# Performance work log

Hardware: AMD Instinct MI355X
Metric: run time of the kernel (lower is better)

## Reference

```python
import jax, jax.numpy as jnp
import numpy as np

B, S, F, H = 256, 1024, 64, 64

def setup_inputs() -> dict:
    key = jax.random.key(0)
    ks = jax.random.split(key, 6)
    x = jax.random.normal(ks[0], (B, S, F), dtype=jnp.float32)
    # Keras LSTM params: kernel [F,4H], recurrent_kernel [H,4H], bias [4H] (gate order i,f,c,o)
    kernel = jax.random.normal(ks[1], (F, 4 * H), dtype=jnp.float32) * (1.0 / np.sqrt(F))
    rec_kernel = jax.random.normal(ks[2], (H, 4 * H), dtype=jnp.float32) * (1.0 / np.sqrt(H))
    bias = jnp.zeros((4 * H,), dtype=jnp.float32)
    dense_w = jax.random.normal(ks[3], (H, 1), dtype=jnp.float32) * (1.0 / np.sqrt(H))
    dense_b = jnp.zeros((1,), dtype=jnp.float32)
    return {"x": x, "kernel": kernel, "rec_kernel": rec_kernel, "bias": bias,
            "dense_w": dense_w, "dense_b": dense_b}

def reference(x, kernel, rec_kernel, bias, dense_w, dense_b):
    # Precompute input contribution for all timesteps: [B,S,4H]
    xz = jnp.einsum('bsf,fg->bsg', x, kernel) + bias
    xz_t = jnp.transpose(xz, (1, 0, 2))  # [S,B,4H]

    def step(carry, xz_step):
        h, c = carry
        z = xz_step + h @ rec_kernel  # [B,4H]
        zi, zf, zc, zo = jnp.split(z, 4, axis=-1)
        i = jax.nn.sigmoid(zi)
        f = jax.nn.sigmoid(zf)
        o = jax.nn.sigmoid(zo)
        c_new = f * c + i * jnp.tanh(zc)
        h_new = o * jnp.tanh(c_new)
        return (h_new, c_new), h_new

    h0 = jnp.zeros((x.shape[0], rec_kernel.shape[0]), dtype=x.dtype)
    c0 = jnp.zeros_like(h0)
    _, hs = jax.lax.scan(step, (h0, c0), xz_t)  # hs: [S,B,H]
    hs = jnp.transpose(hs, (1, 0, 2))  # [B,S,H]
    out = jax.nn.sigmoid(hs @ dense_w + dense_b)  # [B,S,1]
    return out
```

## Files before the change

### kernel.cpp

```cpp
#include <hip/hip_runtime.h>

typedef __attribute__((ext_vector_type(8))) short short8;
typedef __attribute__((ext_vector_type(4))) float f32x4;

#define SS 1024
#define NBLK 64
#define HROW 72

__device__ __forceinline__ float sigmoidf_(float x) {
    return __builtin_amdgcn_rcpf(1.0f + __expf(-x));
}
__device__ __forceinline__ float tanhf_(float x) {
    return 1.0f - 2.0f * __builtin_amdgcn_rcpf(__expf(2.0f * x) + 1.0f);
}
__device__ __forceinline__ unsigned short f2bf(float f) {
    unsigned int u = __float_as_uint(f);
    u += 0x7fffu + ((u >> 16) & 1u);
    return (unsigned short)(u >> 16);
}
__device__ __forceinline__ float bf2f(unsigned short u) {
    return __uint_as_float((unsigned int)u << 16);
}
__device__ __forceinline__ float h2f_lo(unsigned int u) {
    _Float16 h; unsigned short s = (unsigned short)(u & 0xffffu);
    __builtin_memcpy(&h, &s, 2); return (float)h;
}
__device__ __forceinline__ float h2f_hi(unsigned int u) {
    _Float16 h; unsigned short s = (unsigned short)(u >> 16);
    __builtin_memcpy(&h, &s, 2); return (float)h;
}
__device__ __forceinline__ unsigned int pkf16(float a, float b) {
    auto p = __builtin_amdgcn_cvt_pkrtz(a, b);
    unsigned int u; __builtin_memcpy(&u, &p, 4); return u;
}

#define RAW_BARRIER() asm volatile("s_waitcnt lgkmcnt(0)\n\ts_barrier" ::: "memory")

#define MF(A, Bv, C) __builtin_amdgcn_mfma_f32_16x16x32_bf16(A, Bv, C, 0, 0, 0)


#define LOADB(VAR, G, KC, SRC, NN) do {                                       \
    const int kb = ((KC) << 5) + (q << 3);                                    \
    short8 v;                                                                 \
    v[0] = (short)f2bf(SRC[(kb + 0) * 256 + (NN)]);                           \
    v[1] = (short)f2bf(SRC[(kb + 1) * 256 + (NN)]);                           \
    v[2] = (short)f2bf(SRC[(kb + 2) * 256 + (NN)]);                           \
    v[3] = (short)f2bf(SRC[(kb + 3) * 256 + (NN)]);                           \
    v[4] = (short)f2bf(SRC[(kb + 4) * 256 + (NN)]);                           \
    v[5] = (short)f2bf(SRC[(kb + 5) * 256 + (NN)]);                           \
    v[6] = (short)f2bf(SRC[(kb + 6) * 256 + (NN)]);                           \
    v[7] = (short)f2bf(SRC[(kb + 7) * 256 + (NN)]);                           \
    VAR = v; } while (0)

#define CREGION(T, PAR) do {                                                   \
    const short8 ha0 = *(const short8*)&hbuf[(PAR) ^ 1][m * HROW + (q << 3)];  \
    const short8 ha1 = *(const short8*)&hbuf[(PAR) ^ 1][m * HROW + 32 + (q << 3)]; \
    const uint2 cur = ring[(T) & 1][q][n0];                                    \
    const float vi = h2f_lo(cur.x), vf = h2f_hi(cur.x);                        \
    const float vc = h2f_lo(cur.y), vo = h2f_hi(cur.y);                        \
    const f32x4 cgc = {vc, vc, vc, vc};                                        \
    const f32x4 cgo = {vo, vo, vo, vo};                                        \
    const f32x4 cgi = {vi, vi, vi, vi};                                        \
    const f32x4 cgf = {vf, vf, vf, vf};                                        \
    const f32x4 zc = MF(ha1, BHC1, MF(ha0, BHC0, cgc));                        \
    const f32x4 zo = MF(ha1, BHO1, MF(ha0, BHO0, cgo));                        \
    const f32x4 zi = MF(ha1, BHI1, MF(ha0, BHI0, cgi));                        \
    const f32x4 zf = MF(ha1, BHF1, MF(ha0, BHF0, cgf));                        \
    const float tc = tanhf_(zc[0]);                                            \
    const float go = sigmoidf_(zo[0]);                                         \
    const float gi = sigmoidf_(zi[0]);                                         \
    const float gf = sigmoidf_(zf[0]);                                         \
    cc0 = gf * cc0 + gi * tc;                                                  \
    const float h0 = go * tanhf_(cc0);                                         \
    const unsigned short hb16 = f2bf(h0);                                      \
    hbuf[PAR][(q << 2) * HROW + n0] = (short)hb16;                             \
    hb[(size_t)(T) << 6] = hb16;                                               \
    RAW_BARRIER();                                                             \
} while (0)

#define PPROD(S, RPS, F0, F1, F2, F3) do {                                     \
    if ((S) < SS) {                                                            \
        short8 xa0, xa1;                                                       \
        xa0[0] = (short)f2bf(F0.x); xa0[1] = (short)f2bf(F0.y);                \
        xa0[2] = (short)f2bf(F0.z); xa0[3] = (short)f2bf(F0.w);                \
        xa0[4] = (short)f2bf(F1.x); xa0[5] = (short)f2bf(F1.y);                \
        xa0[6] = (short)f2bf(F1.z); xa0[7] = (short)f2bf(F1.w);                \
        xa1[0] = (short)f2bf(F2.x); xa1[1] = (short)f2bf(F2.y);                \
        xa1[2] = (short)f2bf(F2.z); xa1[3] = (short)f2bf(F2.w);                \
        xa1[4] = (short)f2bf(F3.x); xa1[5] = (short)f2bf(F3.y);                \
        xa1[6] = (short)f2bf(F3.z); xa1[7] = (short)f2bf(F3.w);                \
        const f32x4 zi = MF(xa1, WI1, MF(xa0, WI0, cbi));                      \
        const f32x4 zf = MF(xa1, WF1, MF(xa0, WF0, cbf));                      \
        const f32x4 zc = MF(xa1, WC1, MF(xa0, WC0, cbc));                      \
        const f32x4 zo = MF(xa1, WO1, MF(xa0, WO0, cbo));                      \
        uint2 v;                                                               \
        v.x = pkf16(zi[0], zf[0]);                                             \
        v.y = pkf16(zc[0], zo[0]);                                             \
        ring[RPS][q][pw16m] = v;                                               \
    }                                                                          \
    { const int sn = ((S) + 2 < SS) ? (S) + 2 : SS - 1;                        \
      const float* __restrict__ xs = xp + ((size_t)sn << 6);                   \
      F0 = *(const float4*)(xs + (q << 3));                                    \
      F1 = *(const float4*)(xs + (q << 3) + 4);                                \
      F2 = *(const float4*)(xs + 32 + (q << 3));                               \
      F3 = *(const float4*)(xs + 36 + (q << 3)); }                             \
    RAW_BARRIER();                                                             \
} while (0)

__global__ __launch_bounds__(512, 1)
void lstm_fused(const float* __restrict__ x, const float* __restrict__ wk,
                const float* __restrict__ rk, const float* __restrict__ bias,
                unsigned short* __restrict__ hg) {
    const int bb  = blockIdx.x;
    const int tid = threadIdx.x;
    const int l   = tid & 63;
    const int w   = tid >> 6;
    const int m   = l & 15;
    const int q   = l >> 4;

    __shared__ short hbuf[2][16 * HROW];
    __shared__ uint2 ring[2][4][64];

    for (int i = tid; i < 2 * 16 * HROW; i += 512) ((short*)hbuf)[i] = 0;
    __syncthreads();

    if (w < 4) {
        const int n0 = (w << 4) + m;
        short8 BHI0, BHI1, BHF0, BHF1, BHC0, BHC1, BHO0, BHO1;
        LOADB(BHI0, 0, 0, rk, (0 << 6) + n0); LOADB(BHI1, 0, 1, rk, (0 << 6) + n0);
        LOADB(BHF0, 1, 0, rk, (1 << 6) + n0); LOADB(BHF1, 1, 1, rk, (1 << 6) + n0);
        LOADB(BHC0, 2, 0, rk, (2 << 6) + n0); LOADB(BHC1, 2, 1, rk, (2 << 6) + n0);
        LOADB(BHO0, 3, 0, rk, (3 << 6) + n0); LOADB(BHO1, 3, 1, rk, (3 << 6) + n0);

        unsigned short* __restrict__ hb =
            hg + ((size_t)((bb << 2) + q) << 16) + n0;
        float cc0 = 0.f;

        RAW_BARRIER();
        for (int t = 0; t < SS; t += 2) {
            CREGION(t,     0);
            CREGION(t + 1, 1);
        }
    } else {
        const int pw16m = ((w - 4) << 4) + m;
        short8 WI0, WI1, WF0, WF1, WC0, WC1, WO0, WO1;
        LOADB(WI0, 0, 0, wk, (0 << 6) + pw16m); LOADB(WI1, 0, 1, wk, (0 << 6) + pw16m);
        LOADB(WF0, 1, 0, wk, (1 << 6) + pw16m); LOADB(WF1, 1, 1, wk, (1 << 6) + pw16m);
        LOADB(WC0, 2, 0, wk, (2 << 6) + pw16m); LOADB(WC1, 2, 1, wk, (2 << 6) + pw16m);
        LOADB(WO0, 3, 0, wk, (3 << 6) + pw16m); LOADB(WO1, 3, 1, wk, (3 << 6) + pw16m);

        const float bi = bias[(0 << 6) + pw16m];
        const float bf = bias[(1 << 6) + pw16m];
        const float bc = bias[(2 << 6) + pw16m];
        const float bo = bias[(3 << 6) + pw16m];
        const f32x4 cbi = {bi, bi, bi, bi};
        const f32x4 cbf = {bf, bf, bf, bf};
        const f32x4 cbc = {bc, bc, bc, bc};
        const f32x4 cbo = {bo, bo, bo, bo};

        const float* __restrict__ xp =
            x + ((size_t)((bb << 2) + (m >> 2)) << 16);

        float4 XA0 = *(const float4*)(xp + (q << 3));
        float4 XA1 = *(const float4*)(xp + (q << 3) + 4);
        float4 XA2 = *(const float4*)(xp + 32 + (q << 3));
        float4 XA3 = *(const float4*)(xp + 36 + (q << 3));
        float4 XB0 = *(const float4*)(xp + 64 + (q << 3));
        float4 XB1 = *(const float4*)(xp + 64 + (q << 3) + 4);
        float4 XB2 = *(const float4*)(xp + 96 + (q << 3));
        float4 XB3 = *(const float4*)(xp + 100 + (q << 3));

        PPROD(0, 0, XA0, XA1, XA2, XA3);
        for (int t = 0; t < SS; t += 2) {
            PPROD(t + 1, 1, XB0, XB1, XB2, XB3);
            PPROD(t + 2, 0, XA0, XA1, XA2, XA3);
        }
    }
}

__global__ __launch_bounds__(256)
void dense_out(const unsigned short* __restrict__ hg,
               const float* __restrict__ dw, const float* __restrict__ db,
               float* __restrict__ out) {
    const int row = blockIdx.x * 256 + threadIdx.x;
    const short8* __restrict__ hr = (const short8*)(hg + (size_t)row * 64);
    float acc = db[0];
#pragma unroll
    for (int jj = 0; jj < 8; ++jj) {
        const short8 v = hr[jj];
#pragma unroll
        for (int k = 0; k < 8; ++k)
            acc += bf2f((unsigned short)v[k]) * dw[jj * 8 + k];
    }
    out[row] = sigmoidf_(acc);
}

extern "C" void kernel_launch(void* const* d_in, const int* in_sizes, int n_in,
                              void* d_out, int out_size, void* d_ws, size_t ws_size,
                              hipStream_t stream) {
    const float* x    = (const float*)d_in[0];
    const float* wk   = (const float*)d_in[1];
    const float* rk   = (const float*)d_in[2];
    const float* bias = (const float*)d_in[3];
    const float* dw   = (const float*)d_in[4];
    const float* db   = (const float*)d_in[5];
    float* out = (float*)d_out;

    unsigned short* hg = (unsigned short*)d_ws;

    hipLaunchKernelGGL(lstm_fused, dim3(NBLK), dim3(512), 0, stream,
                       x, wk, rk, bias, hg);
    hipLaunchKernelGGL(dense_out, dim3(1024), dim3(256), 0, stream,
                       hg, dw, db, out);
}
```

Measured before the change: 457.3 us.

## Fuse dense output head into LSTM producer warps, drop h workspace and second kernel

Producer warps now compute the final dense projection and sigmoid for each timestep directly from the shared-memory h buffer, using an MFMA against bf16 dense weights. The workers take turns round-robin by step. This removes the global write of all hidden states, the second kernel launch, and the re-read of h. Recurrent warps also get raised scheduling priority. In exchange the producer warps carry extra work inside the latency-critical barrier-synchronised loop, which could slow each step.

```diff
diff --git a/kernel.cpp b/kernel.cpp
--- a/kernel.cpp
+++ b/kernel.cpp
@@ -17,9 +17,6 @@
     unsigned int u = __float_as_uint(f);
     u += 0x7fffu + ((u >> 16) & 1u);
     return (unsigned short)(u >> 16);
-}
-__device__ __forceinline__ float bf2f(unsigned short u) {
-    return __uint_as_float((unsigned int)u << 16);
 }
 __device__ __forceinline__ float h2f_lo(unsigned int u) {
     _Float16 h; unsigned short s = (unsigned short)(u & 0xffffu);
@@ -55,7 +52,7 @@
 #define CREGION(T, PAR) do {                                                   \
     const short8 ha0 = *(const short8*)&hbuf[(PAR) ^ 1][m * HROW + (q << 3)];  \
     const short8 ha1 = *(const short8*)&hbuf[(PAR) ^ 1][m * HROW + 32 + (q << 3)]; \
-    const uint2 cur = ring[(T) & 1][q][n0];                                    \
+    const uint2 cur = ring[PAR][q][n0];                                        \
     const float vi = h2f_lo(cur.x), vf = h2f_hi(cur.x);                        \
     const float vc = h2f_lo(cur.y), vo = h2f_hi(cur.y);                        \
     const f32x4 cgc = {vc, vc, vc, vc};                                        \
@@ -72,14 +69,12 @@
     const float gf = sigmoidf_(zf[0]);                                         \
     cc0 = gf * cc0 + gi * tc;                                                  \
     const float h0 = go * tanhf_(cc0);                                         \
-    const unsigned short hb16 = f2bf(h0);                                      \
-    hbuf[PAR][(q << 2) * HROW + n0] = (short)hb16;                             \
-    hb[(size_t)(T) << 6] = hb16;                                               \
+    hbuf[PAR][(q << 2) * HROW + n0] = (short)f2bf(h0);                         \
     RAW_BARRIER();                                                             \
 } while (0)
 
-#define PPROD(S, RPS, F0, F1, F2, F3) do {                                     \
-    if ((S) < SS) {                                                            \
+#define PCALL(K, RPS, F0, F1, F2, F3) do {                                     \
+    if ((K) < SS) {                                                            \
         short8 xa0, xa1;                                                       \
         xa0[0] = (short)f2bf(F0.x); xa0[1] = (short)f2bf(F0.y);                \
         xa0[2] = (short)f2bf(F0.z); xa0[3] = (short)f2bf(F0.w);                \
@@ -98,7 +93,17 @@
         v.y = pkf16(zc[0], zo[0]);                                             \
         ring[RPS][q][pw16m] = v;                                               \
     }                                                                          \
-    { const int sn = ((S) + 2 < SS) ? (S) + 2 : SS - 1;                        \
+    if ((K) >= 2 && pw == ((K) & 3)) {                 \
+        const short8 da0 = *(const short8*)&hbuf[(K) & 1][m * HROW + (q << 3)];\
+        const short8 da1 = *(const short8*)&hbuf[(K) & 1][m * HROW + 32 + (q << 3)]; \
+        const f32x4 zz = {0.f, 0.f, 0.f, 0.f};                                 \
+        const f32x4 z4 = MF(da1, BD1, MF(da0, BD0, zz));                       \
+        if (m == 0) {                                                          \
+            out[((size_t)((bb << 2) + q) << 10) + (K) - 2] =                   \
+                sigmoidf_(z4[0] + db0);                                        \
+        }                                                                      \
+    }                                                                          \
+    { const int sn = ((K) + 2 < SS) ? (K) + 2 : SS - 1;                        \
       const float* __restrict__ xs = xp + ((size_t)sn << 6);                   \
       F0 = *(const float4*)(xs + (q << 3));                                    \
       F1 = *(const float4*)(xs + (q << 3) + 4);                                \
@@ -110,7 +115,8 @@
 __global__ __launch_bounds__(512, 1)
 void lstm_fused(const float* __restrict__ x, const float* __restrict__ wk,
                 const float* __restrict__ rk, const float* __restrict__ bias,
-                unsigned short* __restrict__ hg) {
+                const float* __restrict__ dw, const float* __restrict__ db,
+                float* __restrict__ out) {
     const int bb  = blockIdx.x;
     const int tid = threadIdx.x;
     const int l   = tid & 63;
@@ -132,17 +138,16 @@
         LOADB(BHC0, 2, 0, rk, (2 << 6) + n0); LOADB(BHC1, 2, 1, rk, (2 << 6) + n0);
         LOADB(BHO0, 3, 0, rk, (3 << 6) + n0); LOADB(BHO1, 3, 1, rk, (3 << 6) + n0);
 
-        unsigned short* __restrict__ hb =
-            hg + ((size_t)((bb << 2) + q) << 16) + n0;
         float cc0 = 0.f;
-
+        __builtin_amdgcn_s_setprio(1);
         RAW_BARRIER();
         for (int t = 0; t < SS; t += 2) {
             CREGION(t,     0);
             CREGION(t + 1, 1);
         }
     } else {
-        const int pw16m = ((w - 4) << 4) + m;
+        const int pw    = w - 4;
+        const int pw16m = (pw << 4) + m;
         short8 WI0, WI1, WF0, WF1, WC0, WC1, WO0, WO1;
         LOADB(WI0, 0, 0, wk, (0 << 6) + pw16m); LOADB(WI1, 0, 1, wk, (0 << 6) + pw16m);
         LOADB(WF0, 1, 0, wk, (1 << 6) + pw16m); LOADB(WF1, 1, 1, wk, (1 << 6) + pw16m);
@@ -158,6 +163,19 @@
         const f32x4 cbc = {bc, bc, bc, bc};
         const f32x4 cbo = {bo, bo, bo, bo};
 
+        short8 BD0, BD1;
+        {
+            short8 v0 = {0, 0, 0, 0, 0, 0, 0, 0}, v1 = v0;
+            if (m == 0) {
+#pragma unroll
+                for (int i = 0; i < 8; ++i) v0[i] = (short)f2bf(dw[(q << 3) + i]);
+#pragma unroll
+                for (int i = 0; i < 8; ++i) v1[i] = (short)f2bf(dw[32 + (q << 3) + i]);
+            }
+            BD0 = v0; BD1 = v1;
+        }
+        const float db0 = db[0];
+
         const float* __restrict__ xp =
             x + ((size_t)((bb << 2) + (m >> 2)) << 16);
 
@@ -170,29 +188,22 @@
         float4 XB2 = *(const float4*)(xp + 96 + (q << 3));
         float4 XB3 = *(const float4*)(xp + 100 + (q << 3));
 
-        PPROD(0, 0, XA0, XA1, XA2, XA3);
-        for (int t = 0; t < SS; t += 2) {
-            PPROD(t + 1, 1, XB0, XB1, XB2, XB3);
-            PPROD(t + 2, 0, XA0, XA1, XA2, XA3);
+        PCALL(0, 0, XA0, XA1, XA2, XA3);
+        for (int k = 1; k < SS; k += 2) {
+            PCALL(k,     1, XB0, XB1, XB2, XB3);
+            PCALL(k + 1, 0, XA0, XA1, XA2, XA3);
+        }
+        if (pw == 1) {
+            const short8 da0 = *(const short8*)&hbuf[1][m * HROW + (q << 3)];
+            const short8 da1 = *(const short8*)&hbuf[1][m * HROW + 32 + (q << 3)];
+            const f32x4 zz = {0.f, 0.f, 0.f, 0.f};
+            const f32x4 z4 = MF(da1, BD1, MF(da0, BD0, zz));
+            if (m == 0) {
+                out[((size_t)((bb << 2) + q) << 10) + SS - 1] =
+                    sigmoidf_(z4[0] + db0);
+            }
         }
     }
-}
-
-__global__ __launch_bounds__(256)
-void dense_out(const unsigned short* __restrict__ hg,
-               const float* __restrict__ dw, const float* __restrict__ db,
-               float* __restrict__ out) {
-    const int row = blockIdx.x * 256 + threadIdx.x;
-    const short8* __restrict__ hr = (const short8*)(hg + (size_t)row * 64);
-    float acc = db[0];
-#pragma unroll
-    for (int jj = 0; jj < 8; ++jj) {
-        const short8 v = hr[jj];
-#pragma unroll
-        for (int k = 0; k < 8; ++k)
-            acc += bf2f((unsigned short)v[k]) * dw[jj * 8 + k];
-    }
-    out[row] = sigmoidf_(acc);
 }
 
 extern "C" void kernel_launch(void* const* d_in, const int* in_sizes, int n_in,
@@ -206,10 +217,6 @@
     const float* db   = (const float*)d_in[5];
     float* out = (float*)d_out;
 
-    unsigned short* hg = (unsigned short*)d_ws;
-
     hipLaunchKernelGGL(lstm_fused, dim3(NBLK), dim3(512), 0, stream,
-                       x, wk, rk, bias, hg);
-    hipLaunchKernelGGL(dense_out, dim3(1024), dim3(256), 0, stream,
-                       hg, dw, db, out);
-}
+                       x, wk, rk, bias, dw, db, out);
+}
```

New measurement: 556.6 us. 1.22x slower.
